# Kernel optimization log

Measured on AMD Instinct MI355X. Metric: run time of the kernel, lower is better.

Reference implementation:

```python
import jax, jax.numpy as jnp
import numpy as np

N_NODES = 100000
N_EDGES = 3200000
IN_CH = 128
HID = 64
N_GRAPHS = 512


def _gcn_conv(x, W, b, src, dst, n_nodes):
    """PyG GCNConv: out = D^{-1/2} (A + I) D^{-1/2} X W + b.
    src/dst are edge endpoints; self-loops handled analytically."""
    h = x @ W  # [N, out]
    # degree with self-loops (count at target nodes, as in PyG)
    deg = jnp.zeros((n_nodes,), h.dtype).at[dst].add(1.0) + 1.0
    dis = jax.lax.rsqrt(deg)  # deg^{-1/2}
    norm = dis[src] * dis[dst]  # [E]
    msg = h[src] * norm[:, None]  # gather + scale, [E, out]
    out = jnp.zeros_like(h).at[dst].add(msg)  # scatter-add
    # self-loop term: norm_ii = 1/deg_i
    out = out + h * (dis * dis)[:, None]
    return out + b


def setup_inputs() -> dict:
    key = jax.random.key(0)
    ks = jax.random.split(key, 8)
    x = jax.random.normal(ks[0], (N_NODES, IN_CH), dtype=jnp.float32)
    edge_index = jax.random.randint(ks[1], (2, N_EDGES), 0, N_NODES, dtype=jnp.int64)
    batch = jnp.sort(jax.random.randint(ks[2], (N_NODES,), 0, N_GRAPHS, dtype=jnp.int64))
    s1 = 1.0 / np.sqrt(IN_CH)
    s2 = 1.0 / np.sqrt(HID)
    W1 = jax.random.uniform(ks[3], (IN_CH, HID), jnp.float32, -s1, s1)
    b1 = jax.random.uniform(ks[4], (HID,), jnp.float32, -s1, s1)
    W2 = jax.random.uniform(ks[5], (HID, HID), jnp.float32, -s2, s2)
    b2 = jax.random.uniform(ks[6], (HID,), jnp.float32, -s2, s2)
    return {"x": x, "edge_index": edge_index, "batch": batch,
            "W1": W1, "b1": b1, "W2": W2, "b2": b2}


def reference(x, edge_index, batch, W1, b1, W2, b2):
    src, dst = edge_index[0], edge_index[1]
    n = x.shape[0]
    h = jax.nn.relu(_gcn_conv(x, W1, b1, src, dst, n))
    h = jax.nn.relu(_gcn_conv(h, W2, b2, src, dst, n))
    # F.dropout(p=0.2) treated as identity (eval / deterministic reference)
    # global_mean_pool: segment mean over graph ids
    sums = jax.ops.segment_sum(h, batch, num_segments=N_GRAPHS)
    cnts = jax.ops.segment_sum(jnp.ones((n,), h.dtype), batch, num_segments=N_GRAPHS)
    return sums / jnp.maximum(cnts, 1.0)[:, None]
```

## Files before the change

### kernel.cpp

```cpp
#include <hip/hip_runtime.h>

typedef unsigned int uint;

#define N_NODES 100000
#define N_EDGES 3200000
#define IN_CH 128
#define HID 64
#define N_GRAPHS 512
#define EPB 4096
#define NBLK ((N_EDGES + EPB - 1) / EPB)
#define NB 391

__device__ __forceinline__ uint f2bf1(float f) {
    union { float f; uint i; } v; v.f = f;
    return (v.i + 0x7fffu + ((v.i >> 16) & 1u)) >> 16;
}
__device__ __forceinline__ uint pack2(float lo, float hi) {
    return f2bf1(lo) | (f2bf1(hi) << 16);
}
__device__ __forceinline__ void bacc(uint u, float& lo, float& hi) {
    union { uint i; float f; } t0, t1;
    t0.i = u << 16;
    t1.i = u & 0xffff0000u;
    lo += t0.f; hi += t1.f;
}

__global__ __launch_bounds__(256) void binhist_kernel(const int* __restrict__ dst,
                                                      int* __restrict__ hist_g) {
    __shared__ int h[4 * NB];
    for (int i = threadIdx.x; i < 4 * NB; i += 256) h[i] = 0;
    __syncthreads();
    int w = threadIdx.x >> 6;
    int base = blockIdx.x * EPB;
    int end = min(base + EPB, N_EDGES);
    for (int e = base + threadIdx.x; e < end; e += 256)
        atomicAdd(&h[w * NB + (dst[e] >> 8)], 1);
    __syncthreads();
    for (int b = threadIdx.x; b < NB; b += 256)
        hist_g[b * NBLK + blockIdx.x] = h[b] + h[NB + b] + h[2 * NB + b] + h[3 * NB + b];
}

__global__ __launch_bounds__(256) void s1_kernel(int* __restrict__ hist_g,
                                                 int* __restrict__ total) {
    __shared__ int buf[NBLK];
    int b = blockIdx.x;
    for (int j = threadIdx.x; j < NBLK; j += 256) buf[j] = hist_g[b * NBLK + j];
    __syncthreads();
    if (threadIdx.x == 0) {
        int run = 0;
        for (int j = 0; j < NBLK; ++j) { int v = buf[j]; buf[j] = run; run += v; }
        total[b] = run;
    }
    __syncthreads();
    for (int j = threadIdx.x; j < NBLK; j += 256) hist_g[b * NBLK + j] = buf[j];
}

__global__ __launch_bounds__(512) void s2_kernel(const int* __restrict__ total,
                                                 int* __restrict__ bbase) {
    __shared__ int s[512];
    int t = threadIdx.x;
    int v = (t < NB) ? total[t] : 0;
    s[t] = v;
    __syncthreads();
#pragma unroll
    for (int o = 1; o < 512; o <<= 1) {
        int x = (t >= o) ? s[t - o] : 0;
        __syncthreads();
        s[t] += x;
        __syncthreads();
    }
    if (t < NB) bbase[t] = s[t] - v;
    if (t == 0) bbase[NB] = N_EDGES;
}

__global__ __launch_bounds__(256) void binscatter_kernel(const int* __restrict__ src,
                                                         const int* __restrict__ dst,
                                                         const int* __restrict__ hist_g,
                                                         const int* __restrict__ bbase,
                                                         uint* __restrict__ pairs) {
    __shared__ int cur[NB];
    __shared__ int start[NB];
    for (int i = threadIdx.x; i < NB; i += 256) {
        cur[i] = 0;
        start[i] = bbase[i] + hist_g[i * NBLK + blockIdx.x];
    }
    __syncthreads();
    int base = blockIdx.x * EPB;
    int end = min(base + EPB, N_EDGES);
    for (int e = base + threadIdx.x; e < end; e += 256) {
        int s = src[e], d = dst[e];
        int b = d >> 8;
        int r = atomicAdd(&cur[b], 1);
        pairs[start[b] + r] = ((uint)(d & 255) << 24) | (uint)s;
    }
}

__global__ __launch_bounds__(256) void bucket_csr_kernel(const uint* __restrict__ pairs,
                                                         const int* __restrict__ bbase,
                                                         int* __restrict__ csr_src,
                                                         int* __restrict__ row_ptr,
                                                         float* __restrict__ dis) {
    __shared__ int h[256];
    int b = blockIdx.x;
    int t = threadIdx.x;
    int e0 = bbase[b];
    int e1 = bbase[b + 1];
    h[t] = 0;
    __syncthreads();
    for (int e = e0 + t; e < e1; e += 256)
        atomicAdd(&h[pairs[e] >> 24], 1);
    __syncthreads();
    int v = h[t];
#pragma unroll
    for (int o = 1; o < 256; o <<= 1) {
        int x = (t >= o) ? h[t - o] : 0;
        __syncthreads();
        h[t] += x;
        __syncthreads();
    }
    int excl = h[t] - v;
    int n = b * 256 + t;
    if (n < N_NODES) {
        row_ptr[n] = e0 + excl;
        dis[n] = rsqrtf((float)v + 1.0f);
    }
    if (b == NB - 1 && t == 0) row_ptr[N_NODES] = N_EDGES;
    __syncthreads();
    h[t] = e0 + excl;
    __syncthreads();
    for (int e = e0 + t; e < e1; e += 256) {
        uint p = pairs[e];
        int pos = atomicAdd(&h[p >> 24], 1);
        csr_src[pos] = (int)(p & 0xFFFFFFu);
    }
}

template<int K, bool RELU>
__global__ __launch_bounds__(256) void gemm_kernel(const float* __restrict__ X,
                                                   const float* __restrict__ W,
                                                   const float* __restrict__ dis,
                                                   uint* __restrict__ Y) {
    __shared__ float Wl[K * 64];
    int t = threadIdx.x;
    for (int idx = t; idx < K * 64; idx += 256) Wl[idx] = W[idx];
    __syncthreads();

    int row = blockIdx.x * 32 + (t >> 3);
    if (row >= N_NODES) return;
    int c0 = (t & 7) * 8;

    float acc[8] = {0.f, 0.f, 0.f, 0.f, 0.f, 0.f, 0.f, 0.f};
    const float* xr = X + (size_t)row * K;
#pragma unroll 8
    for (int k = 0; k < K; k += 4) {
        float4 xv = *reinterpret_cast<const float4*>(xr + k);
        if (RELU) {
            xv.x = fmaxf(xv.x, 0.f); xv.y = fmaxf(xv.y, 0.f);
            xv.z = fmaxf(xv.z, 0.f); xv.w = fmaxf(xv.w, 0.f);
        }
        float xk[4] = {xv.x, xv.y, xv.z, xv.w};
#pragma unroll
        for (int kk = 0; kk < 4; ++kk) {
            const float4 w0 = *reinterpret_cast<const float4*>(&Wl[(k + kk) * 64 + c0]);
            const float4 w1 = *reinterpret_cast<const float4*>(&Wl[(k + kk) * 64 + c0 + 4]);
            acc[0] += xk[kk] * w0.x; acc[1] += xk[kk] * w0.y;
            acc[2] += xk[kk] * w0.z; acc[3] += xk[kk] * w0.w;
            acc[4] += xk[kk] * w1.x; acc[5] += xk[kk] * w1.y;
            acc[6] += xk[kk] * w1.z; acc[7] += xk[kk] * w1.w;
        }
    }
    float d = dis[row];
    uint4 o;
    o.x = pack2(acc[0] * d, acc[1] * d);
    o.y = pack2(acc[2] * d, acc[3] * d);
    o.z = pack2(acc[4] * d, acc[5] * d);
    o.w = pack2(acc[6] * d, acc[7] * d);
    *reinterpret_cast<uint4*>(Y + (size_t)row * 32 + (t & 7) * 4) = o;
}

__global__ __launch_bounds__(256) void gather_kernel(const int* __restrict__ row_ptr,
                                                     const int* __restrict__ csr_src,
                                                     const float* __restrict__ dis,
                                                     const float* __restrict__ bias,
                                                     const uint* __restrict__ A,
                                                     float* __restrict__ B) {
    int i = blockIdx.x * 4 + (threadIdx.x >> 6);
    if (i >= N_NODES) return;
    int lane = threadIdx.x & 63;
    int q = lane >> 4;
    int cu = (lane & 15) * 2;

    int e = row_ptr[i];
    int end = row_ptr[i + 1];

    float a0 = 0.f, a1 = 0.f, a2 = 0.f, a3 = 0.f;
    float b0 = 0.f, b1 = 0.f, b2 = 0.f, b3 = 0.f;
    if (q == 0) {
        uint2 u = *reinterpret_cast<const uint2*>(&A[(size_t)i * 32 + cu]);
        bacc(u.x, a0, a1); bacc(u.y, a2, a3);
    }
    for (; e + 8 <= end; e += 8) {
        int s0 = csr_src[e + q];
        int s1 = csr_src[e + 4 + q];
        uint2 u0 = *reinterpret_cast<const uint2*>(&A[(size_t)s0 * 32 + cu]);
        uint2 u1 = *reinterpret_cast<const uint2*>(&A[(size_t)s1 * 32 + cu]);
        bacc(u0.x, a0, a1); bacc(u0.y, a2, a3);
        bacc(u1.x, b0, b1); bacc(u1.y, b2, b3);
    }
    for (; e + 4 <= end; e += 4) {
        int s = csr_src[e + q];
        uint2 u = *reinterpret_cast<const uint2*>(&A[(size_t)s * 32 + cu]);
        bacc(u.x, a0, a1); bacc(u.y, a2, a3);
    }
    if (e + q < end) {
        int s = csr_src[e + q];
        uint2 u = *reinterpret_cast<const uint2*>(&A[(size_t)s * 32 + cu]);
        bacc(u.x, b0, b1); bacc(u.y, b2, b3);
    }
    a0 += b0; a1 += b1; a2 += b2; a3 += b3;

    a0 += __shfl_xor(a0, 16); a0 += __shfl_xor(a0, 32);
    a1 += __shfl_xor(a1, 16); a1 += __shfl_xor(a1, 32);
    a2 += __shfl_xor(a2, 16); a2 += __shfl_xor(a2, 32);
    a3 += __shfl_xor(a3, 16); a3 += __shfl_xor(a3, 32);

    if (q == 0) {
        int c4 = (lane & 15) * 4;
        float d = dis[i];
        float4 o;
        o.x = bias[c4]     + d * a0;
        o.y = bias[c4 + 1] + d * a1;
        o.z = bias[c4 + 2] + d * a2;
        o.w = bias[c4 + 3] + d * a3;
        *reinterpret_cast<float4*>(&B[(size_t)i * 64 + c4]) = o;
    }
}

__global__ __launch_bounds__(256) void pool_kernel(const float* __restrict__ B,
                                                   const int* __restrict__ batch,
                                                   float* __restrict__ sums,
                                                   float* __restrict__ cnt) {
    int w = blockIdx.x * 4 + (threadIdx.x >> 6);
    int lane = threadIdx.x & 63;
    int n0 = w * 32;
    if (n0 >= N_NODES) return;
    int n1 = min(n0 + 32, N_NODES);
    int curg = batch[n0];
    float acc = 0.f;
    int run = 0;
    for (int n = n0; n < n1; ++n) {
        int g = batch[n];
        if (g != curg) {
            atomicAdd(&sums[curg * 64 + lane], acc);
            if (lane == 0) atomicAdd(&cnt[curg], (float)run);
            curg = g; acc = 0.f; run = 0;
        }
        acc += fmaxf(B[(size_t)n * 64 + lane], 0.f);
        run++;
    }
    atomicAdd(&sums[curg * 64 + lane], acc);
    if (lane == 0) atomicAdd(&cnt[curg], (float)run);
}

__global__ __launch_bounds__(256) void final_kernel(const float* __restrict__ sums,
                                                    const float* __restrict__ cnt,
                                                    float* __restrict__ out) {
    int idx = blockIdx.x * 256 + threadIdx.x;
    if (idx < N_GRAPHS * 64) out[idx] = sums[idx] / fmaxf(cnt[idx >> 6], 1.0f);
}

extern "C" void kernel_launch(void* const* d_in, const int* in_sizes, int n_in,
                              void* d_out, int out_size, void* d_ws, size_t ws_size,
                              hipStream_t stream) {
    const float* x     = (const float*)d_in[0];
    const int*   edge  = (const int*)d_in[1];
    const int*   batch = (const int*)d_in[2];
    const float* W1    = (const float*)d_in[3];
    const float* b1    = (const float*)d_in[4];
    const float* W2    = (const float*)d_in[5];
    const float* b2    = (const float*)d_in[6];
    float* out = (float*)d_out;

    uint*  A        = (uint*)d_ws;
    float* B        = (float*)(A + (size_t)N_NODES * 32);
    float* dis      = B + (size_t)N_NODES * 64;
    float* sums     = dis + N_NODES;
    float* cnt_f    = sums + (size_t)N_GRAPHS * 64;
    int*   row_ptr  = (int*)(cnt_f + N_GRAPHS);
    int*   hist_g   = row_ptr + N_NODES + 1;
    int*   total    = hist_g + NB * NBLK;
    int*   bbase    = total + NB;
    int*   csr_src  = bbase + NB + 1;
    uint*  pairs    = A;

    const int* src = edge;
    const int* dst = edge + N_EDGES;

    hipMemsetAsync(sums, 0, (N_GRAPHS * 64 + N_GRAPHS) * sizeof(float), stream);

    binhist_kernel<<<NBLK, 256, 0, stream>>>(dst, hist_g);
    s1_kernel<<<NB, 256, 0, stream>>>(hist_g, total);
    s2_kernel<<<1, 512, 0, stream>>>(total, bbase);
    binscatter_kernel<<<NBLK, 256, 0, stream>>>(src, dst, hist_g, bbase, pairs);
    bucket_csr_kernel<<<NB, 256, 0, stream>>>(pairs, bbase, csr_src, row_ptr, dis);

    gemm_kernel<IN_CH, false><<<(N_NODES + 31) / 32, 256, 0, stream>>>(x, W1, dis, A);
    gather_kernel<<<(N_NODES + 3) / 4, 256, 0, stream>>>(row_ptr, csr_src, dis, b1, A, B);

    gemm_kernel<HID, true><<<(N_NODES + 31) / 32, 256, 0, stream>>>(B, W2, dis, A);
    gather_kernel<<<(N_NODES + 3) / 4, 256, 0, stream>>>(row_ptr, csr_src, dis, b2, A, B);

    pool_kernel<<<(N_NODES + 127) / 128, 256, 0, stream>>>(B, batch, sums, cnt_f);
    final_kernel<<<(N_GRAPHS * 64 + 255) / 256, 256, 0, stream>>>(sums, cnt_f, out);
}
```

Measured before the change: 401.1 us.

## Fuse edge binning into one atomic-reservation pass, retile GEMM, widen gather

```diff
diff --git a/kernel.cpp b/kernel.cpp
--- a/kernel.cpp
+++ b/kernel.cpp
@@ -10,6 +10,7 @@
 #define EPB 4096
 #define NBLK ((N_EDGES + EPB - 1) / EPB)
 #define NB 391
+#define CAP 10240
 
 __device__ __forceinline__ uint f2bf1(float f) {
     union { float f; uint i; } v; v.f = f;
@@ -25,86 +26,58 @@
     lo += t0.f; hi += t1.f;
 }
 
-__global__ __launch_bounds__(256) void binhist_kernel(const int* __restrict__ dst,
-                                                      int* __restrict__ hist_g) {
+__global__ __launch_bounds__(256) void scatter_kernel(const int* __restrict__ src,
+                                                      const int* __restrict__ dst,
+                                                      int* __restrict__ bcnt,
+                                                      uint* __restrict__ pairs) {
     __shared__ int h[4 * NB];
-    for (int i = threadIdx.x; i < 4 * NB; i += 256) h[i] = 0;
-    __syncthreads();
-    int w = threadIdx.x >> 6;
+    __shared__ int start[NB];
+    __shared__ int cur[NB];
+    int t = threadIdx.x;
     int base = blockIdx.x * EPB;
-    int end = min(base + EPB, N_EDGES);
-    for (int e = base + threadIdx.x; e < end; e += 256)
-        atomicAdd(&h[w * NB + (dst[e] >> 8)], 1);
-    __syncthreads();
-    for (int b = threadIdx.x; b < NB; b += 256)
-        hist_g[b * NBLK + blockIdx.x] = h[b] + h[NB + b] + h[2 * NB + b] + h[3 * NB + b];
-}
-
-__global__ __launch_bounds__(256) void s1_kernel(int* __restrict__ hist_g,
-                                                 int* __restrict__ total) {
-    __shared__ int buf[NBLK];
-    int b = blockIdx.x;
-    for (int j = threadIdx.x; j < NBLK; j += 256) buf[j] = hist_g[b * NBLK + j];
-    __syncthreads();
-    if (threadIdx.x == 0) {
-        int run = 0;
-        for (int j = 0; j < NBLK; ++j) { int v = buf[j]; buf[j] = run; run += v; }
-        total[b] = run;
-    }
-    __syncthreads();
-    for (int j = threadIdx.x; j < NBLK; j += 256) hist_g[b * NBLK + j] = buf[j];
-}
-
-__global__ __launch_bounds__(512) void s2_kernel(const int* __restrict__ total,
-                                                 int* __restrict__ bbase) {
-    __shared__ int s[512];
-    int t = threadIdx.x;
-    int v = (t < NB) ? total[t] : 0;
-    s[t] = v;
-    __syncthreads();
-#pragma unroll
-    for (int o = 1; o < 512; o <<= 1) {
-        int x = (t >= o) ? s[t - o] : 0;
-        __syncthreads();
-        s[t] += x;
-        __syncthreads();
-    }
-    if (t < NB) bbase[t] = s[t] - v;
-    if (t == 0) bbase[NB] = N_EDGES;
-}
-
-__global__ __launch_bounds__(256) void binscatter_kernel(const int* __restrict__ src,
-                                                         const int* __restrict__ dst,
-                                                         const int* __restrict__ hist_g,
-                                                         const int* __restrict__ bbase,
-                                                         uint* __restrict__ pairs) {
-    __shared__ int cur[NB];
-    __shared__ int start[NB];
-    for (int i = threadIdx.x; i < NB; i += 256) {
-        cur[i] = 0;
-        start[i] = bbase[i] + hist_g[i * NBLK + blockIdx.x];
-    }
-    __syncthreads();
-    int base = blockIdx.x * EPB;
-    int end = min(base + EPB, N_EDGES);
-    for (int e = base + threadIdx.x; e < end; e += 256) {
-        int s = src[e], d = dst[e];
-        int b = d >> 8;
-        int r = atomicAdd(&cur[b], 1);
-        pairs[start[b] + r] = ((uint)(d & 255) << 24) | (uint)s;
+
+    int rs[16], rd[16];
+#pragma unroll
+    for (int j = 0; j < 16; ++j) {
+        int e = base + j * 256 + t;
+        if (e < N_EDGES) { rs[j] = src[e]; rd[j] = dst[e]; }
+        else rd[j] = -1;
+    }
+    for (int i = t; i < 4 * NB; i += 256) h[i] = 0;
+    __syncthreads();
+    int w = t >> 6;
+#pragma unroll
+    for (int j = 0; j < 16; ++j)
+        if (rd[j] >= 0) atomicAdd(&h[w * NB + (rd[j] >> 8)], 1);
+    __syncthreads();
+    for (int b = t; b < NB; b += 256) {
+        int tot = h[b] + h[NB + b] + h[2 * NB + b] + h[3 * NB + b];
+        start[b] = tot ? atomicAdd(&bcnt[b * 16], tot) : 0;
+        cur[b] = 0;
+    }
+    __syncthreads();
+#pragma unroll
+    for (int j = 0; j < 16; ++j) {
+        if (rd[j] >= 0) {
+            int b = rd[j] >> 8;
+            int r = atomicAdd(&cur[b], 1);
+            pairs[(size_t)b * CAP + start[b] + r] =
+                ((uint)(rd[j] & 255) << 24) | (uint)rs[j];
+        }
     }
 }
 
 __global__ __launch_bounds__(256) void bucket_csr_kernel(const uint* __restrict__ pairs,
-                                                         const int* __restrict__ bbase,
+                                                         const int* __restrict__ bcnt,
                                                          int* __restrict__ csr_src,
-                                                         int* __restrict__ row_ptr,
+                                                         int* __restrict__ rstart,
+                                                         int* __restrict__ rend,
                                                          float* __restrict__ dis) {
     __shared__ int h[256];
     int b = blockIdx.x;
     int t = threadIdx.x;
-    int e0 = bbase[b];
-    int e1 = bbase[b + 1];
+    int e0 = b * CAP;
+    int e1 = e0 + bcnt[b * 16];
     h[t] = 0;
     __syncthreads();
     for (int e = e0 + t; e < e1; e += 256)
@@ -121,10 +94,10 @@
     int excl = h[t] - v;
     int n = b * 256 + t;
     if (n < N_NODES) {
-        row_ptr[n] = e0 + excl;
+        rstart[n] = e0 + excl;
+        rend[n] = e0 + excl + v;
         dis[n] = rsqrtf((float)v + 1.0f);
     }
-    if (b == NB - 1 && t == 0) row_ptr[N_NODES] = N_EDGES;
     __syncthreads();
     h[t] = e0 + excl;
     __syncthreads();
@@ -141,44 +114,72 @@
                                                    const float* __restrict__ dis,
                                                    uint* __restrict__ Y) {
     __shared__ float Wl[K * 64];
+    __shared__ float Xs[128 * 33];
     int t = threadIdx.x;
     for (int idx = t; idx < K * 64; idx += 256) Wl[idx] = W[idx];
-    __syncthreads();
-
-    int row = blockIdx.x * 32 + (t >> 3);
-    if (row >= N_NODES) return;
+
+    int r0 = (t >> 3) * 4;
     int c0 = (t & 7) * 8;
-
-    float acc[8] = {0.f, 0.f, 0.f, 0.f, 0.f, 0.f, 0.f, 0.f};
-    const float* xr = X + (size_t)row * K;
-#pragma unroll 8
-    for (int k = 0; k < K; k += 4) {
-        float4 xv = *reinterpret_cast<const float4*>(xr + k);
-        if (RELU) {
-            xv.x = fmaxf(xv.x, 0.f); xv.y = fmaxf(xv.y, 0.f);
-            xv.z = fmaxf(xv.z, 0.f); xv.w = fmaxf(xv.w, 0.f);
-        }
-        float xk[4] = {xv.x, xv.y, xv.z, xv.w};
-#pragma unroll
-        for (int kk = 0; kk < 4; ++kk) {
-            const float4 w0 = *reinterpret_cast<const float4*>(&Wl[(k + kk) * 64 + c0]);
-            const float4 w1 = *reinterpret_cast<const float4*>(&Wl[(k + kk) * 64 + c0 + 4]);
-            acc[0] += xk[kk] * w0.x; acc[1] += xk[kk] * w0.y;
-            acc[2] += xk[kk] * w0.z; acc[3] += xk[kk] * w0.w;
-            acc[4] += xk[kk] * w1.x; acc[5] += xk[kk] * w1.y;
-            acc[6] += xk[kk] * w1.z; acc[7] += xk[kk] * w1.w;
-        }
-    }
-    float d = dis[row];
-    uint4 o;
-    o.x = pack2(acc[0] * d, acc[1] * d);
-    o.y = pack2(acc[2] * d, acc[3] * d);
-    o.z = pack2(acc[4] * d, acc[5] * d);
-    o.w = pack2(acc[6] * d, acc[7] * d);
-    *reinterpret_cast<uint4*>(Y + (size_t)row * 32 + (t & 7) * 4) = o;
-}
-
-__global__ __launch_bounds__(256) void gather_kernel(const int* __restrict__ row_ptr,
+    int rowBase = blockIdx.x * 128;
+
+    float acc[4][8];
+#pragma unroll
+    for (int a = 0; a < 4; ++a)
+#pragma unroll
+        for (int c = 0; c < 8; ++c) acc[a][c] = 0.f;
+
+    int srow = t >> 1;
+    int shh = (t & 1) * 16;
+    bool sok = (rowBase + srow) < N_NODES;
+    const float* xbase = X + (size_t)(rowBase + srow) * K + shh;
+
+    for (int kc = 0; kc < K; kc += 32) {
+        __syncthreads();
+#pragma unroll
+        for (int f = 0; f < 4; ++f) {
+            float4 v = sok ? *reinterpret_cast<const float4*>(xbase + kc + f * 4)
+                           : make_float4(0.f, 0.f, 0.f, 0.f);
+            if (RELU) {
+                v.x = fmaxf(v.x, 0.f); v.y = fmaxf(v.y, 0.f);
+                v.z = fmaxf(v.z, 0.f); v.w = fmaxf(v.w, 0.f);
+            }
+            int o = srow * 33 + shh + f * 4;
+            Xs[o] = v.x; Xs[o + 1] = v.y; Xs[o + 2] = v.z; Xs[o + 3] = v.w;
+        }
+        __syncthreads();
+#pragma unroll
+        for (int kk = 0; kk < 32; ++kk) {
+            const float4 wa = *reinterpret_cast<const float4*>(&Wl[(kc + kk) * 64 + c0]);
+            const float4 wb = *reinterpret_cast<const float4*>(&Wl[(kc + kk) * 64 + c0 + 4]);
+            float xr[4];
+#pragma unroll
+            for (int a = 0; a < 4; ++a) xr[a] = Xs[(r0 + a) * 33 + kk];
+#pragma unroll
+            for (int a = 0; a < 4; ++a) {
+                acc[a][0] += xr[a] * wa.x; acc[a][1] += xr[a] * wa.y;
+                acc[a][2] += xr[a] * wa.z; acc[a][3] += xr[a] * wa.w;
+                acc[a][4] += xr[a] * wb.x; acc[a][5] += xr[a] * wb.y;
+                acc[a][6] += xr[a] * wb.z; acc[a][7] += xr[a] * wb.w;
+            }
+        }
+    }
+#pragma unroll
+    for (int a = 0; a < 4; ++a) {
+        int row = rowBase + r0 + a;
+        if (row < N_NODES) {
+            float d = dis[row];
+            uint4 o;
+            o.x = pack2(acc[a][0] * d, acc[a][1] * d);
+            o.y = pack2(acc[a][2] * d, acc[a][3] * d);
+            o.z = pack2(acc[a][4] * d, acc[a][5] * d);
+            o.w = pack2(acc[a][6] * d, acc[a][7] * d);
+            *reinterpret_cast<uint4*>(Y + (size_t)row * 32 + (t & 7) * 4) = o;
+        }
+    }
+}
+
+__global__ __launch_bounds__(256) void gather_kernel(const int* __restrict__ rstart,
+                                                     const int* __restrict__ rend,
                                                      const int* __restrict__ csr_src,
                                                      const float* __restrict__ dis,
                                                      const float* __restrict__ bias,
@@ -187,52 +188,62 @@
     int i = blockIdx.x * 4 + (threadIdx.x >> 6);
     if (i >= N_NODES) return;
     int lane = threadIdx.x & 63;
-    int q = lane >> 4;
-    int cu = (lane & 15) * 2;
-
-    int e = row_ptr[i];
-    int end = row_ptr[i + 1];
-
-    float a0 = 0.f, a1 = 0.f, a2 = 0.f, a3 = 0.f;
-    float b0 = 0.f, b1 = 0.f, b2 = 0.f, b3 = 0.f;
+    int q = lane >> 3;
+    int cu = (lane & 7) * 4;
+
+    float4 bi0 = *reinterpret_cast<const float4*>(&bias[(lane & 7) * 8]);
+    float4 bi1 = *reinterpret_cast<const float4*>(&bias[(lane & 7) * 8 + 4]);
+
+    int e = rstart[i];
+    int end = rend[i];
+
+    float a[8], b[8];
+#pragma unroll
+    for (int j = 0; j < 8; ++j) { a[j] = 0.f; b[j] = 0.f; }
+
     if (q == 0) {
-        uint2 u = *reinterpret_cast<const uint2*>(&A[(size_t)i * 32 + cu]);
-        bacc(u.x, a0, a1); bacc(u.y, a2, a3);
+        uint4 u = *reinterpret_cast<const uint4*>(&A[(size_t)i * 32 + cu]);
+        bacc(u.x, a[0], a[1]); bacc(u.y, a[2], a[3]);
+        bacc(u.z, a[4], a[5]); bacc(u.w, a[6], a[7]);
+    }
+    for (; e + 16 <= end; e += 16) {
+        int s0 = csr_src[e + q];
+        int s1 = csr_src[e + 8 + q];
+        uint4 u0 = *reinterpret_cast<const uint4*>(&A[(size_t)s0 * 32 + cu]);
+        uint4 u1 = *reinterpret_cast<const uint4*>(&A[(size_t)s1 * 32 + cu]);
+        bacc(u0.x, a[0], a[1]); bacc(u0.y, a[2], a[3]);
+        bacc(u0.z, a[4], a[5]); bacc(u0.w, a[6], a[7]);
+        bacc(u1.x, b[0], b[1]); bacc(u1.y, b[2], b[3]);
+        bacc(u1.z, b[4], b[5]); bacc(u1.w, b[6], b[7]);
     }
     for (; e + 8 <= end; e += 8) {
-        int s0 = csr_src[e + q];
-        int s1 = csr_src[e + 4 + q];
-        uint2 u0 = *reinterpret_cast<const uint2*>(&A[(size_t)s0 * 32 + cu]);
-        uint2 u1 = *reinterpret_cast<const uint2*>(&A[(size_t)s1 * 32 + cu]);
-        bacc(u0.x, a0, a1); bacc(u0.y, a2, a3);
-        bacc(u1.x, b0, b1); bacc(u1.y, b2, b3);
-    }
-    for (; e + 4 <= end; e += 4) {
         int s = csr_src[e + q];
-        uint2 u = *reinterpret_cast<const uint2*>(&A[(size_t)s * 32 + cu]);
-        bacc(u.x, a0, a1); bacc(u.y, a2, a3);
+        uint4 u = *reinterpret_cast<const uint4*>(&A[(size_t)s * 32 + cu]);
+        bacc(u.x, a[0], a[1]); bacc(u.y, a[2], a[3]);
+        bacc(u.z, a[4], a[5]); bacc(u.w, a[6], a[7]);
     }
     if (e + q < end) {
         int s = csr_src[e + q];
-        uint2 u = *reinterpret_cast<const uint2*>(&A[(size_t)s * 32 + cu]);
-        bacc(u.x, b0, b1); bacc(u.y, b2, b3);
-    }
-    a0 += b0; a1 += b1; a2 += b2; a3 += b3;
-
-    a0 += __shfl_xor(a0, 16); a0 += __shfl_xor(a0, 32);
-    a1 += __shfl_xor(a1, 16); a1 += __shfl_xor(a1, 32);
-    a2 += __shfl_xor(a2, 16); a2 += __shfl_xor(a2, 32);
-    a3 += __shfl_xor(a3, 16); a3 += __shfl_xor(a3, 32);
-
+        uint4 u = *reinterpret_cast<const uint4*>(&A[(size_t)s * 32 + cu]);
+        bacc(u.x, b[0], b[1]); bacc(u.y, b[2], b[3]);
+        bacc(u.z, b[4], b[5]); bacc(u.w, b[6], b[7]);
+    }
+#pragma unroll
+    for (int j = 0; j < 8; ++j) {
+        a[j] += b[j];
+        a[j] += __shfl_xor(a[j], 8);
+        a[j] += __shfl_xor(a[j], 16);
+        a[j] += __shfl_xor(a[j], 32);
+    }
     if (q == 0) {
-        int c4 = (lane & 15) * 4;
         float d = dis[i];
-        float4 o;
-        o.x = bias[c4]     + d * a0;
-        o.y = bias[c4 + 1] + d * a1;
-        o.z = bias[c4 + 2] + d * a2;
-        o.w = bias[c4 + 3] + d * a3;
-        *reinterpret_cast<float4*>(&B[(size_t)i * 64 + c4]) = o;
+        float* br = B + (size_t)i * 64 + (lane & 7) * 8;
+        *reinterpret_cast<float4*>(br) =
+            make_float4(bi0.x + d * a[0], bi0.y + d * a[1],
+                        bi0.z + d * a[2], bi0.w + d * a[3]);
+        *reinterpret_cast<float4*>(br + 4) =
+            make_float4(bi1.x + d * a[4], bi1.y + d * a[5],
+                        bi1.z + d * a[6], bi1.w + d * a[7]);
     }
 }
 
@@ -282,33 +293,29 @@
     float* out = (float*)d_out;
 
     uint*  A        = (uint*)d_ws;
-    float* B        = (float*)(A + (size_t)N_NODES * 32);
-    float* dis      = B + (size_t)N_NODES * 64;
-    float* sums     = dis + N_NODES;
+    int*   csr_src  = (int*)(A + (size_t)N_NODES * 32);
+    float* dis      = (float*)(csr_src + NB * CAP);
+    int*   rstart   = (int*)(dis + N_NODES);
+    int*   rend     = rstart + N_NODES;
+    float* sums     = (float*)(rend + N_NODES);
     float* cnt_f    = sums + (size_t)N_GRAPHS * 64;
-    int*   row_ptr  = (int*)(cnt_f + N_GRAPHS);
-    int*   hist_g   = row_ptr + N_NODES + 1;
-    int*   total    = hist_g + NB * NBLK;
-    int*   bbase    = total + NB;
-    int*   csr_src  = bbase + NB + 1;
-    uint*  pairs    = A;
+    int*   bcnt     = (int*)(cnt_f + N_GRAPHS);
+    float* B        = (float*)(bcnt + NB * 16);
+    uint*  pairs    = (uint*)B;
 
     const int* src = edge;
     const int* dst = edge + N_EDGES;
 
-    hipMemsetAsync(sums, 0, (N_GRAPHS * 64 + N_GRAPHS) * sizeof(float), stream);
-
-    binhist_kernel<<<NBLK, 256, 0, stream>>>(dst, hist_g);
-    s1_kernel<<<NB, 256, 0, stream>>>(hist_g, total);
-    s2_kernel<<<1, 512, 0, stream>>>(total, bbase);
-    binscatter_kernel<<<NBLK, 256, 0, stream>>>(src, dst, hist_g, bbase, pairs);
-    bucket_csr_kernel<<<NB, 256, 0, stream>>>(pairs, bbase, csr_src, row_ptr, dis);
-
-    gemm_kernel<IN_CH, false><<<(N_NODES + 31) / 32, 256, 0, stream>>>(x, W1, dis, A);
-    gather_kernel<<<(N_NODES + 3) / 4, 256, 0, stream>>>(row_ptr, csr_src, dis, b1, A, B);
-
-    gemm_kernel<HID, true><<<(N_NODES + 31) / 32, 256, 0, stream>>>(B, W2, dis, A);
-    gather_kernel<<<(N_NODES + 3) / 4, 256, 0, stream>>>(row_ptr, csr_src, dis, b2, A, B);
+    hipMemsetAsync(sums, 0, (N_GRAPHS * 64 + N_GRAPHS + NB * 16) * sizeof(float), stream);
+
+    scatter_kernel<<<NBLK, 256, 0, stream>>>(src, dst, bcnt, pairs);
+    bucket_csr_kernel<<<NB, 256, 0, stream>>>(pairs, bcnt, csr_src, rstart, rend, dis);
+
+    gemm_kernel<IN_CH, false><<<(N_NODES + 127) / 128, 256, 0, stream>>>(x, W1, dis, A);
+    gather_kernel<<<(N_NODES + 3) / 4, 256, 0, stream>>>(rstart, rend, csr_src, dis, b1, A, B);
+
+    gemm_kernel<HID, true><<<(N_NODES + 127) / 128, 256, 0, stream>>>(B, W2, dis, A);
+    gather_kernel<<<(N_NODES + 3) / 4, 256, 0, stream>>>(rstart, rend, csr_src, dis, b2, A, B);
 
     pool_kernel<<<(N_NODES + 127) / 128, 256, 0, stream>>>(B, batch, sums, cnt_f);
     final_kernel<<<(N_GRAPHS * 64 + 255) / 256, 256, 0, stream>>>(sums, cnt_f, out);
```

Measured after the change: 370.2 us. 7.7% less time.
